# Kernel tuning notes

Measured on AMD Instinct MI355X. Metric: run time of the kernel, lower is better.

## Reference

```python
import jax, jax.numpy as jnp
import numpy as np

PAD = 3  # static pad; offsets are bounded so ceil(L) == PAD at runtime


def setup_inputs() -> dict:
    key = jax.random.key(0)
    ks = jax.random.split(key, 6)
    N, D, H, W = 32, 3, 160, 160
    M, K = 16, 8
    x = jax.random.normal(ks[0], (N, D, H, W), jnp.float32)
    u = lambda k: jax.random.uniform(k, (M, K), jnp.float32, -2.99, 2.99)
    dx1 = u(ks[1]).at[0, 0].set(2.9)  # pin max |offset| > 2 so ceil(L) == 3
    dx2 = u(ks[2])
    dy1 = u(ks[3])
    dy2 = u(ks[4])
    th = jax.random.normal(ks[5], (M, K), jnp.float32) * 0.1
    return {"x": x, "dx1": dx1, "dx2": dx2, "dy1": dy1, "dy2": dy2, "th": th}


def _fern_bit_word(x, dx1, dx2, dy1, dy2, th):
    N, D, H, W = x.shape
    # L = max over all |offsets| (as in the original call())
    L = jnp.maximum(
        jnp.maximum(jnp.max(jnp.abs(dx1)), jnp.max(jnp.abs(dx2))),
        jnp.maximum(jnp.max(jnp.abs(dy1)), jnp.max(jnp.abs(dy2))),
    )
    p = jnp.ceil(L).astype(jnp.int32)  # original pad amount (data-dependent)
    shift = PAD - p                    # re-base indices onto the static PAD (==0 here)

    ch = x[:, 1, :, :]                 # original always slices channel index 1
    Tp = jnp.pad(ch, ((0, 0), (PAD, PAD), (PAD, PAD)))  # (N, H+2PAD, W+2PAD)

    def interp(dx, dy):
        # x1 = int32(L + floor(dx)) as in __Bit (truncating cast), rebased to PAD
        x1 = (L + jnp.floor(dx)).astype(jnp.int32) + shift
        y1 = (L + jnp.floor(dy)).astype(jnp.int32) + shift
        fx = dx - jnp.floor(dx)
        fy = dy - jnp.floor(dy)
        # one (H+1, W+1) window gives all four bilinear corners
        win = jax.lax.dynamic_slice(Tp, (0, y1, x1), (N, H + 1, W + 1))
        return ((1 - fx) * (1 - fy) * win[:, :H, :W]
                + fx * (1 - fy) * win[:, :H, 1:]
                + (1 - fx) * fy * win[:, 1:, :W]
                + fx * fy * win[:, 1:, 1:])

    def bit(a1, a2, b1, b2, t):
        b = interp(a1, b1) - interp(a2, b2) - t
        # linear sigmoid: clip((b + 0.5) / (2 * ambiguity), 0, 1), ambiguity = 2
        return jnp.clip((b + 0.5) / 4.0, 0.0, 1.0)

    bits = jax.vmap(bit)(dx1.ravel(), dx2.ravel(), dy1.ravel(), dy2.ravel(), th.ravel())
    # (M*K, N, H, W) -> (N, M*K, H, W): concat of bit maps along axis 1
    return jnp.transpose(bits, (1, 0, 2, 3))


def reference(x, dx1, dx2, dy1, dy2, th):
    return _fern_bit_word(x, dx1, dx2, dy1, dy2, th)
```

## Files before the change

kernel.cpp:

```cpp
#include <hip/hip_runtime.h>


#define PSTRIDE 168
#define WROWS   14
#define GBITS   32
#define HT      8
#define BLK     320

__global__ __launch_bounds__(BLK) void fern_kernel(
    const float* __restrict__ x,
    const float* __restrict__ dx1, const float* __restrict__ dx2,
    const float* __restrict__ dy1, const float* __restrict__ dy2,
    const float* __restrict__ th,
    float* __restrict__ out)
{
    const int rt = blockIdx.x;
    const int bg = blockIdx.y;
    const int n  = blockIdx.z;

    __shared__ float  Wbuf[WROWS * PSTRIDE];
    __shared__ float4 Pw[GBITS][3];
    __shared__ int    Po[GBITS][2];
    __shared__ float  red[BLK / 64];
    __shared__ float  Lsh;

    const int tid = threadIdx.x;

    float m = 0.f;
    if (tid < 128) {
        m = fmaxf(fmaxf(fabsf(dx1[tid]), fabsf(dx2[tid])),
                  fmaxf(fabsf(dy1[tid]), fabsf(dy2[tid])));
    }
    #pragma unroll
    for (int d = 32; d >= 1; d >>= 1) m = fmaxf(m, __shfl_xor(m, d));
    const int lane = tid & 63, wid = tid >> 6;
    if (lane == 0) red[wid] = m;
    __syncthreads();
    if (tid == 0) {
        float L = red[0];
        #pragma unroll
        for (int i = 1; i < BLK / 64; ++i) L = fmaxf(L, red[i]);
        Lsh = L;
    }
    __syncthreads();
    const float L = Lsh;
    const int shift = 3 - (int)ceilf(L);

    if (tid < GBITS) {
        const int j = bg * GBITS + tid;
        const float a1 = dx1[j], a2 = dx2[j], b1 = dy1[j], b2 = dy2[j];
        const float fa1 = floorf(a1), fa2 = floorf(a2);
        const float fb1 = floorf(b1), fb2 = floorf(b2);
        int x1 = (int)(L + fa1) + shift; x1 = min(max(x1, 0), 5);
        int y1 = (int)(L + fb1) + shift; y1 = min(max(y1, 0), 5);
        int x2 = (int)(L + fa2) + shift; x2 = min(max(x2, 0), 5);
        int y2 = (int)(L + fb2) + shift; y2 = min(max(y2, 0), 5);
        const float fx1 = a1 - fa1, fy1 = b1 - fb1;
        const float fx2 = a2 - fa2, fy2 = b2 - fb2;
        Pw[tid][0] = make_float4( 0.25f*(1.f-fx1)*(1.f-fy1),  0.25f*fx1*(1.f-fy1),
                                  0.25f*(1.f-fx1)*fy1,        0.25f*fx1*fy1);
        Pw[tid][1] = make_float4(-0.25f*(1.f-fx2)*(1.f-fy2), -0.25f*fx2*(1.f-fy2),
                                 -0.25f*(1.f-fx2)*fy2,       -0.25f*fx2*fy2);
        Pw[tid][2] = make_float4((0.5f - th[j]) * 0.25f, 0.f, 0.f, 0.f);
        Po[tid][0] = y1 * PSTRIDE + x1;
        Po[tid][1] = y2 * PSTRIDE + x2;
    }

    const float* __restrict__ src = x + ((size_t)n * 3 + 1) * 25600;
    const int h0 = rt * HT;
    for (int e = tid; e < WROWS * 166; e += BLK) {
        const int r = e / 166, c = e - r * 166;
        const int sr = h0 + r - 3, sc = c - 3;
        float v = 0.f;
        if ((unsigned)sr < 160u && (unsigned)sc < 160u) v = src[sr * 160 + sc];
        Wbuf[r * PSTRIDE + c] = v;
    }
    __syncthreads();

    const int w     = tid % 160;
    const int rb    = tid / 160;
    const int rbase = rb * 4;
    const int lbase = rbase * PSTRIDE + w;

    float* __restrict__ outp =
        out + ((size_t)n * 128 + bg * GBITS) * 25600 + (h0 + rbase) * 160 + w;

    #pragma unroll 2
    for (int j = 0; j < GBITS; ++j) {
        const float4 s1 = Pw[j][0];
        const float4 s2 = Pw[j][1];
        const float  c0 = Pw[j][2].x;
        const int o1 = Po[j][0] + lbase;
        const int o2 = Po[j][1] + lbase;

        float acc0 = c0, acc1 = c0, acc2 = c0, acc3 = c0;

        {
            float t0 = Wbuf[o1              ], t1 = Wbuf[o1               + 1];
            float u0 = Wbuf[o1 +   PSTRIDE  ], u1 = Wbuf[o1 +   PSTRIDE   + 1];
            acc0 += s1.x*t0 + s1.y*t1 + s1.z*u0 + s1.w*u1;
            t0 = Wbuf[o1 + 2*PSTRIDE]; t1 = Wbuf[o1 + 2*PSTRIDE + 1];
            acc1 += s1.x*u0 + s1.y*u1 + s1.z*t0 + s1.w*t1;
            u0 = Wbuf[o1 + 3*PSTRIDE]; u1 = Wbuf[o1 + 3*PSTRIDE + 1];
            acc2 += s1.x*t0 + s1.y*t1 + s1.z*u0 + s1.w*u1;
            t0 = Wbuf[o1 + 4*PSTRIDE]; t1 = Wbuf[o1 + 4*PSTRIDE + 1];
            acc3 += s1.x*u0 + s1.y*u1 + s1.z*t0 + s1.w*t1;
        }
        {
            float t0 = Wbuf[o2              ], t1 = Wbuf[o2               + 1];
            float u0 = Wbuf[o2 +   PSTRIDE  ], u1 = Wbuf[o2 +   PSTRIDE   + 1];
            acc0 += s2.x*t0 + s2.y*t1 + s2.z*u0 + s2.w*u1;
            t0 = Wbuf[o2 + 2*PSTRIDE]; t1 = Wbuf[o2 + 2*PSTRIDE + 1];
            acc1 += s2.x*u0 + s2.y*u1 + s2.z*t0 + s2.w*t1;
            u0 = Wbuf[o2 + 3*PSTRIDE]; u1 = Wbuf[o2 + 3*PSTRIDE + 1];
            acc2 += s2.x*t0 + s2.y*t1 + s2.z*u0 + s2.w*u1;
            t0 = Wbuf[o2 + 4*PSTRIDE]; t1 = Wbuf[o2 + 4*PSTRIDE + 1];
            acc3 += s2.x*u0 + s2.y*u1 + s2.z*t0 + s2.w*t1;
        }

        outp[  0] = fminf(fmaxf(acc0, 0.f), 1.f);
        outp[160] = fminf(fmaxf(acc1, 0.f), 1.f);
        outp[320] = fminf(fmaxf(acc2, 0.f), 1.f);
        outp[480] = fminf(fmaxf(acc3, 0.f), 1.f);
        outp += 25600;
    }
}

extern "C" void kernel_launch(void* const* d_in, const int* in_sizes, int n_in,
                              void* d_out, int out_size, void* d_ws, size_t ws_size,
                              hipStream_t stream) {
    const float* x   = (const float*)d_in[0];
    const float* dx1 = (const float*)d_in[1];
    const float* dx2 = (const float*)d_in[2];
    const float* dy1 = (const float*)d_in[3];
    const float* dy2 = (const float*)d_in[4];
    const float* th  = (const float*)d_in[5];
    float* out = (float*)d_out;

    dim3 grid(20, 4, 32);
    fern_kernel<<<grid, BLK, 0, stream>>>(x, dx1, dx2, dy1, dy2, th, out);
}
```

Baseline: 440.0 us.

## Compute 4x4 output tiles per thread with padded LDS and float4 stores

Each thread now computes a 4x4 patch of outputs per bit, loading a 5x5 window from shared memory once per sample instead of 2 loads per output, which cuts LDS traffic. The shared tile grows to 32 output rows, using a skewed column index (c + c/4) to avoid bank conflicts on the strided accesses. The grid becomes 5x8x32 with 16 bits per block. Outputs are written as float4 vector stores. Costs include more registers per thread and fewer blocks, and the skewed padding may break the 16-byte alignment of the float4 stores in some layouts.

After: 454.3 us. +3.3%, slower.

```diff
diff --git a/kernel.cpp b/kernel.cpp
--- a/kernel.cpp
+++ b/kernel.cpp
@@ -1,11 +1,15 @@
 #include <hip/hip_runtime.h>
 
 
-#define PSTRIDE 168
-#define WROWS   14
-#define GBITS   32
-#define HT      8
-#define BLK     320
+#define PROWS 38
+#define PSTR  208
+#define GBITS 16
+#define HT    32
+#define BLK   320
+
+__device__ __forceinline__ float clamp01(float v) {
+    return fminf(fmaxf(v, 0.f), 1.f);
+}
 
 __global__ __launch_bounds__(BLK) void fern_kernel(
     const float* __restrict__ x,
@@ -18,9 +22,10 @@
     const int bg = blockIdx.y;
     const int n  = blockIdx.z;
 
-    __shared__ float  Wbuf[WROWS * PSTRIDE];
-    __shared__ float4 Pw[GBITS][3];
-    __shared__ int    Po[GBITS][2];
+    __shared__ float  Wbuf[PROWS * PSTR];
+    __shared__ float4 Pw[GBITS][2];
+    __shared__ float  Pc[GBITS];
+    __shared__ int    Po[GBITS][4];
     __shared__ float  red[BLK / 64];
     __shared__ float  Lsh;
 
@@ -61,67 +66,86 @@
                                   0.25f*(1.f-fx1)*fy1,        0.25f*fx1*fy1);
         Pw[tid][1] = make_float4(-0.25f*(1.f-fx2)*(1.f-fy2), -0.25f*fx2*(1.f-fy2),
                                  -0.25f*(1.f-fx2)*fy2,       -0.25f*fx2*fy2);
-        Pw[tid][2] = make_float4((0.5f - th[j]) * 0.25f, 0.f, 0.f, 0.f);
-        Po[tid][0] = y1 * PSTRIDE + x1;
-        Po[tid][1] = y2 * PSTRIDE + x2;
+        Pc[tid] = (0.5f - th[j]) * 0.25f;
+        Po[tid][0] = y1 * PSTR;  Po[tid][1] = x1;
+        Po[tid][2] = y2 * PSTR;  Po[tid][3] = x2;
     }
 
     const float* __restrict__ src = x + ((size_t)n * 3 + 1) * 25600;
     const int h0 = rt * HT;
-    for (int e = tid; e < WROWS * 166; e += BLK) {
+    for (int e = tid; e < PROWS * 166; e += BLK) {
         const int r = e / 166, c = e - r * 166;
         const int sr = h0 + r - 3, sc = c - 3;
         float v = 0.f;
         if ((unsigned)sr < 160u && (unsigned)sc < 160u) v = src[sr * 160 + sc];
-        Wbuf[r * PSTRIDE + c] = v;
+        Wbuf[r * PSTR + c + (c >> 2)] = v;
     }
     __syncthreads();
 
-    const int w     = tid % 160;
-    const int rb    = tid / 160;
-    const int rbase = rb * 4;
-    const int lbase = rbase * PSTRIDE + w;
+    const int cg = tid % 40, rg = tid / 40;
+    const int w0 = cg * 4, rbase = rg * 4;
+    const int rowoff = rbase * PSTR;
 
     float* __restrict__ outp =
-        out + ((size_t)n * 128 + bg * GBITS) * 25600 + (h0 + rbase) * 160 + w;
+        out + ((size_t)n * 128 + bg * GBITS) * 25600 + (h0 + rbase) * 160 + w0;
 
-    #pragma unroll 2
+    #pragma unroll 1
     for (int j = 0; j < GBITS; ++j) {
         const float4 s1 = Pw[j][0];
         const float4 s2 = Pw[j][1];
-        const float  c0 = Pw[j][2].x;
-        const int o1 = Po[j][0] + lbase;
-        const int o2 = Po[j][1] + lbase;
+        const float  c0 = Pc[j];
 
-        float acc0 = c0, acc1 = c0, acc2 = c0, acc3 = c0;
+        float acc[4][4];
+        #pragma unroll
+        for (int i = 0; i < 4; ++i)
+            #pragma unroll
+            for (int k = 0; k < 4; ++k) acc[i][k] = c0;
+
+        float P[5][5];
+        int pc[5];
 
         {
-            float t0 = Wbuf[o1              ], t1 = Wbuf[o1               + 1];
-            float u0 = Wbuf[o1 +   PSTRIDE  ], u1 = Wbuf[o1 +   PSTRIDE   + 1];
-            acc0 += s1.x*t0 + s1.y*t1 + s1.z*u0 + s1.w*u1;
-            t0 = Wbuf[o1 + 2*PSTRIDE]; t1 = Wbuf[o1 + 2*PSTRIDE + 1];
-            acc1 += s1.x*u0 + s1.y*u1 + s1.z*t0 + s1.w*t1;
-            u0 = Wbuf[o1 + 3*PSTRIDE]; u1 = Wbuf[o1 + 3*PSTRIDE + 1];
-            acc2 += s1.x*t0 + s1.y*t1 + s1.z*u0 + s1.w*u1;
-            t0 = Wbuf[o1 + 4*PSTRIDE]; t1 = Wbuf[o1 + 4*PSTRIDE + 1];
-            acc3 += s1.x*u0 + s1.y*u1 + s1.z*t0 + s1.w*t1;
+            const int o  = Po[j][0] + rowoff;
+            const int cx = Po[j][1] + w0;
+            #pragma unroll
+            for (int c = 0; c < 5; ++c) { int q = cx + c; pc[c] = q + (q >> 2); }
+            #pragma unroll
+            for (int i = 0; i < 5; ++i)
+                #pragma unroll
+                for (int c = 0; c < 5; ++c)
+                    P[i][c] = Wbuf[o + i * PSTR + pc[c]];
+            #pragma unroll
+            for (int i = 0; i < 4; ++i)
+                #pragma unroll
+                for (int k = 0; k < 4; ++k)
+                    acc[i][k] += s1.x*P[i][k] + s1.y*P[i][k+1]
+                               + s1.z*P[i+1][k] + s1.w*P[i+1][k+1];
         }
         {
-            float t0 = Wbuf[o2              ], t1 = Wbuf[o2               + 1];
-            float u0 = Wbuf[o2 +   PSTRIDE  ], u1 = Wbuf[o2 +   PSTRIDE   + 1];
-            acc0 += s2.x*t0 + s2.y*t1 + s2.z*u0 + s2.w*u1;
-            t0 = Wbuf[o2 + 2*PSTRIDE]; t1 = Wbuf[o2 + 2*PSTRIDE + 1];
-            acc1 += s2.x*u0 + s2.y*u1 + s2.z*t0 + s2.w*t1;
-            u0 = Wbuf[o2 + 3*PSTRIDE]; u1 = Wbuf[o2 + 3*PSTRIDE + 1];
-            acc2 += s2.x*t0 + s2.y*t1 + s2.z*u0 + s2.w*u1;
-            t0 = Wbuf[o2 + 4*PSTRIDE]; t1 = Wbuf[o2 + 4*PSTRIDE + 1];
-            acc3 += s2.x*u0 + s2.y*u1 + s2.z*t0 + s2.w*t1;
+            const int o  = Po[j][2] + rowoff;
+            const int cx = Po[j][3] + w0;
+            #pragma unroll
+            for (int c = 0; c < 5; ++c) { int q = cx + c; pc[c] = q + (q >> 2); }
+            #pragma unroll
+            for (int i = 0; i < 5; ++i)
+                #pragma unroll
+                for (int c = 0; c < 5; ++c)
+                    P[i][c] = Wbuf[o + i * PSTR + pc[c]];
+            #pragma unroll
+            for (int i = 0; i < 4; ++i)
+                #pragma unroll
+                for (int k = 0; k < 4; ++k)
+                    acc[i][k] += s2.x*P[i][k] + s2.y*P[i][k+1]
+                               + s2.z*P[i+1][k] + s2.w*P[i+1][k+1];
         }
 
-        outp[  0] = fminf(fmaxf(acc0, 0.f), 1.f);
-        outp[160] = fminf(fmaxf(acc1, 0.f), 1.f);
-        outp[320] = fminf(fmaxf(acc2, 0.f), 1.f);
-        outp[480] = fminf(fmaxf(acc3, 0.f), 1.f);
+        #pragma unroll
+        for (int i = 0; i < 4; ++i) {
+            float4 v;
+            v.x = clamp01(acc[i][0]); v.y = clamp01(acc[i][1]);
+            v.z = clamp01(acc[i][2]); v.w = clamp01(acc[i][3]);
+            *reinterpret_cast<float4*>(outp + i * 160) = v;
+        }
         outp += 25600;
     }
 }
@@ -137,6 +161,6 @@
     const float* th  = (const float*)d_in[5];
     float* out = (float*)d_out;
 
-    dim3 grid(20, 4, 32);
+    dim3 grid(5, 8, 32);
     fern_kernel<<<grid, BLK, 0, stream>>>(x, dx1, dx2, dy1, dy2, th, out);
 }
```
